# Performance work log

Hardware: AMD Instinct MI355X
Metric: run time of the kernel (lower is better)

The kernel has to match this reference:

```python
import jax, jax.numpy as jnp
import numpy as np

EPS = 1e-8
MARGIN = 0.2
LAMBDA_SM_LSE = 6.0   # i2t attention smooth (opt.lambda_softmax_lse)
LAMBDA_SM_AVG = 9.0   # t2i attention smooth (opt.lambda_softmax_avg)
LAMBDA_LSE = 6.0      # LogSumExp aggregation temperature
NEG = -1e9


def _l2norm(x, axis):
    return x / (jnp.sqrt(jnp.sum(x * x, axis=axis, keepdims=True)) + EPS)


def _cos(a, b):
    # cosine over last axis, torch-style: w12 / clamp(|a||b|, eps)
    w12 = jnp.sum(a * b, axis=-1)
    w1 = jnp.sqrt(jnp.sum(a * a, axis=-1))
    w2 = jnp.sqrt(jnp.sum(b * b, axis=-1))
    return w12 / jnp.maximum(w1 * w2, EPS)


def _forward(im, s, s_l):
    B, R, D = im.shape
    W = s.shape[1]
    wmask = jnp.arange(W)[None, :] < s_l[:, None]          # (Bc, W) valid words
    s = s * wmask[:, :, None]                              # emulate ragged slice s[j,:len_j]

    # ---------------- i2t: query=image regions, context=caption words ----------
    # attn[i,j,w,r] = <s[j,w], im[i,r]>
    A = jnp.einsum('jwd,ird->ijwr', s, im)
    A = jax.nn.leaky_relu(A, 0.1)
    A = _l2norm(A, axis=3)                                 # clipped_l2norm over regions
    logits = jnp.swapaxes(A, 2, 3) * LAMBDA_SM_LSE         # (i,j,r,w), softmax over words
    logits = jnp.where(wmask[None, :, None, :], logits, NEG)
    attn_i2t = jax.nn.softmax(logits, axis=-1)
    wc_t = jnp.einsum('ijrw,jwd->ijrd', attn_i2t, s)       # weighted caption ctx per region
    sim1 = _cos(im[:, None, :, :], wc_t)                   # (i,j,r)
    score1 = jnp.log(jnp.sum(jnp.exp(LAMBDA_LSE * sim1), axis=2)) / LAMBDA_LSE  # (i,j)
    attn_t_full = jnp.mean(wc_t, axis=2)                   # (i,j,d)
    idx = jnp.arange(B)
    attn_t = attn_t_full[idx, idx]                         # (B,d) diagonal

    # ---------------- t2i: query=caption words, context=image regions ----------
    # attn[i,j,r,w] = <im[i,r], s[j,w]>
    Bm = jnp.einsum('ird,jwd->ijrw', im, s)
    Bm = jax.nn.leaky_relu(Bm, 0.1)
    Bm = Bm * wmask[None, :, None, :]                      # padded-word cols excluded from norm
    Bm = _l2norm(Bm, axis=3)                               # clipped_l2norm over words
    logits2 = jnp.swapaxes(Bm, 2, 3) * LAMBDA_SM_AVG       # (i,j,w,r), softmax over regions
    attn_t2i = jax.nn.softmax(logits2, axis=-1)
    wc_i = jnp.einsum('ijwr,ird->ijwd', attn_t2i, im)      # weighted image ctx per word
    sim2 = _cos(s[None, :, :, :], wc_i)                    # (i,j,w)
    e2 = jnp.where(wmask[None, :, :], jnp.exp(LAMBDA_LSE * sim2), 0.0)
    score2 = jnp.log(jnp.sum(e2, axis=2)) / LAMBDA_LSE     # masked LogSumExp over words
    wsum = jnp.sum(wc_i * wmask[None, :, :, None], axis=2)
    attn_i_full = wsum / s_l[None, :, None].astype(wc_i.dtype)  # masked mean over words
    attn_i = attn_i_full[idx, idx]                         # (B,d)

    # ---------------- hinge loss over (B,B) score matrix -----------------------
    scores = 0.5 * (score1 + score2)
    diag = jnp.diagonal(scores)
    cost_s = jnp.maximum(MARGIN + scores - diag[:, None], 0.0)
    cost_im = jnp.maximum(MARGIN + scores - diag[None, :], 0.0)
    eye = jnp.eye(B, dtype=bool)
    cost_s = jnp.where(eye, 0.0, cost_s)
    cost_im = jnp.where(eye, 0.0, cost_im)
    # max_violation=True
    loss = jnp.sum(jnp.max(cost_s, axis=1)) + jnp.sum(jnp.max(cost_im, axis=0))
    return loss, attn_t, attn_i


def setup_inputs() -> dict:
    key = jax.random.key(0)
    k1, k2, k3 = jax.random.split(key, 3)
    B, R, W, D = 64, 36, 40, 1024
    im = jax.random.normal(k1, (B, R, D), dtype=jnp.float32)
    s = jax.random.normal(k2, (B, W, D), dtype=jnp.float32)
    s_l = jax.random.randint(k3, (B,), 10, W + 1)
    return {"im": im, "s": s, "s_l": s_l}


def reference(im, s, s_l):
    return _forward(im, s, s_l)
```

## Files before the change

kernel.cpp:

```cpp
#include <hip/hip_runtime.h>
#include <math.h>

#define Bn 64
#define Rr 36
#define Ww 40
#define Dd 1024
#define GM 2304
#define GN 2560
#define NCONV 4864
#define PAD 72
#define SBP 64
#define EPSf 1e-8f

typedef unsigned short u16;
typedef __attribute__((ext_vector_type(8))) short bf16x8;
typedef __attribute__((ext_vector_type(4))) float f32x4;

struct alignas(8) U16x4 { u16 x, y, z, w; };

__device__ inline u16 f2bf(float x) {
    unsigned int u = __float_as_uint(x);
    u += 0x7FFFu + ((u >> 16) & 1u);
    return (u16)(u >> 16);
}
__device__ inline float bf2f(u16 h) {
    return __uint_as_float(((unsigned int)h) << 16);
}

__device__ __forceinline__ void gl_lds16(const u16* g, u16* l) {
    __builtin_amdgcn_global_load_lds(
        (const __attribute__((address_space(1))) void*)g,
        (__attribute__((address_space(3))) void*)l, 16, 0, 0);
}

__global__ __launch_bounds__(256) void prep_kernel(const float* __restrict__ im,
                                                   const float* __restrict__ s,
                                                   const int* __restrict__ s_l,
                                                   u16* __restrict__ Ab,
                                                   u16* __restrict__ Bb,
                                                   u16* __restrict__ SSb,
                                                   u16* __restrict__ IIb,
                                                   float* __restrict__ SSd,
                                                   float* __restrict__ IId) {
    __shared__ float red[3][64][37];
    int b = blockIdx.x, t = threadIdx.x;
    if (b < NCONV) {
        const int nA4 = GM * Dd / 4;
        int idx = b * 256 + t;
        if (idx < nA4) {
            float4 v = *(const float4*)(im + (size_t)idx * 4);
            U16x4 o = {f2bf(v.x), f2bf(v.y), f2bf(v.z), f2bf(v.w)};
            *(U16x4*)(Ab + (size_t)idx * 4) = o;
        } else {
            int i2 = idx - nA4;
            int f = i2 * 4;
            int row = f >> 10;
            int j = row / Ww, w = row - j * Ww;
            U16x4 o = {0, 0, 0, 0};
            if (w < s_l[j]) {
                float4 v = *(const float4*)(s + (size_t)f);
                o.x = f2bf(v.x); o.y = f2bf(v.y); o.z = f2bf(v.z); o.w = f2bf(v.w);
            }
            *(U16x4*)(Bb + (size_t)i2 * 4) = o;
        }
        return;
    }
    int gb = b - NCONV;
    bool isS = gb < Bn;
    int idx = isS ? gb : gb - Bn;
    int n = isS ? Ww : Rr;
    const float* basef = isS ? (s + (size_t)idx * Ww * Dd) : (im + (size_t)idx * Rr * Dd);
    u16* outb = isS ? (SSb + (size_t)idx * 48 * SBP) : (IIb + (size_t)idx * 48 * SBP);
    float* outd = isS ? (SSd + (size_t)idx * Ww) : (IId + (size_t)idx * Rr);
    int lane = t & 63, wid = t >> 6;
    int frow = lane & 15, fk = (lane >> 4) * 8;

    f32x4 acc[3][3];
    for (int m = 0; m < 3; ++m)
        for (int p = 0; p < 3; ++p) acc[m][p] = (f32x4){0.f, 0.f, 0.f, 0.f};

    for (int ks = 0; ks < 8; ++ks) {
        int k0 = wid * 256 + ks * 32 + fk;
        bf16x8 f[3];
        for (int m = 0; m < 3; ++m) {
            int rr = m * 16 + frow;
            if (rr >= n) rr = n - 1;
            const float* p = basef + (size_t)rr * Dd + k0;
            float4 v0 = *(const float4*)p;
            float4 v1 = *(const float4*)(p + 4);
            bf16x8 fv;
            fv[0] = (short)f2bf(v0.x); fv[1] = (short)f2bf(v0.y);
            fv[2] = (short)f2bf(v0.z); fv[3] = (short)f2bf(v0.w);
            fv[4] = (short)f2bf(v1.x); fv[5] = (short)f2bf(v1.y);
            fv[6] = (short)f2bf(v1.z); fv[7] = (short)f2bf(v1.w);
            f[m] = fv;
        }
        for (int m = 0; m < 3; ++m)
            for (int p = 0; p < 3; ++p)
                acc[m][p] = __builtin_amdgcn_mfma_f32_16x16x32_bf16(f[m], f[p], acc[m][p], 0, 0, 0);
    }
    if (wid) {
        for (int m = 0; m < 3; ++m)
            for (int p = 0; p < 3; ++p)
                for (int q = 0; q < 4; ++q)
                    red[wid - 1][lane][(m * 3 + p) * 4 + q] = acc[m][p][q];
    }
    __syncthreads();
    if (wid == 0) {
        for (int wv = 0; wv < 3; ++wv)
            for (int m = 0; m < 3; ++m)
                for (int p = 0; p < 3; ++p)
                    for (int q = 0; q < 4; ++q)
                        acc[m][p][q] += red[wv][lane][(m * 3 + p) * 4 + q];
        int crow = (lane >> 4) * 4, ccol = lane & 15;
        for (int m = 0; m < 3; ++m)
            for (int p = 0; p < 3; ++p)
                for (int q = 0; q < 4; ++q) {
                    int row = m * 16 + crow + q;
                    int col = p * 16 + ccol;
                    float v = acc[m][p][q];
                    outb[row * SBP + col] = f2bf(v);
                    if (row == col && row < n) outd[row] = v;
                }
    }
}

__global__ __launch_bounds__(256) void gemm_mfma_kernel(const u16* __restrict__ Ab,
                                                        const u16* __restrict__ Bb,
                                                        u16* __restrict__ Gb) {
    __shared__ __align__(16) u16 As[2][64][64];
    __shared__ __align__(16) u16 Bs[2][128][64];
    int bn = blockIdx.x;
    int bm = blockIdx.y;
    int t = threadIdx.x;
    int lane = t & 63, wid = t >> 6;
    int wr = wid >> 1, wc = wid & 1;

    int lrow8 = lane >> 3;
    int sslot = (lane & 7) ^ lrow8;
    const u16* ga = Ab + ((size_t)(bm * 64 + wid * 16) + lrow8) * Dd + sslot * 8;
    const u16* gb = Bb + ((size_t)(bn * 128 + wid * 32) + lrow8) * Dd + sslot * 8;

    f32x4 acc[2][4];
    for (int m = 0; m < 2; ++m)
        for (int n = 0; n < 4; ++n) acc[m][n] = (f32x4){0.f, 0.f, 0.f, 0.f};

    int frow = lane & 15;
    int cgr = lane >> 4;

#define STAGE(BI, KK) do { \
        gl_lds16(ga + (KK), &As[BI][wid * 16][0]); \
        gl_lds16(ga + (size_t)8 * Dd + (KK), &As[BI][wid * 16 + 8][0]); \
        gl_lds16(gb + (KK), &Bs[BI][wid * 32][0]); \
        gl_lds16(gb + (size_t)8 * Dd + (KK), &Bs[BI][wid * 32 + 8][0]); \
        gl_lds16(gb + (size_t)16 * Dd + (KK), &Bs[BI][wid * 32 + 16][0]); \
        gl_lds16(gb + (size_t)24 * Dd + (KK), &Bs[BI][wid * 32 + 24][0]); \
    } while (0)

    STAGE(0, 0);
    for (int step = 0; step < 16; ++step) {
        int cur = step & 1;
        __syncthreads();
        if (step < 15) STAGE(cur ^ 1, (step + 1) * 64);
        bf16x8 af[2][2], bf[4][2];
#pragma unroll
        for (int m = 0; m < 2; ++m) {
            int row = wr * 32 + m * 16 + frow;
#pragma unroll
            for (int ks = 0; ks < 2; ++ks) {
                int slot = (ks * 4 + cgr) ^ (row & 7);
                af[m][ks] = *(const bf16x8*)&As[cur][row][slot * 8];
            }
        }
#pragma unroll
        for (int n = 0; n < 4; ++n) {
            int row = wc * 64 + n * 16 + frow;
#pragma unroll
            for (int ks = 0; ks < 2; ++ks) {
                int slot = (ks * 4 + cgr) ^ (row & 7);
                bf[n][ks] = *(const bf16x8*)&Bs[cur][row][slot * 8];
            }
        }
#pragma unroll
        for (int ks = 0; ks < 2; ++ks)
#pragma unroll
            for (int m = 0; m < 2; ++m)
#pragma unroll
                for (int n = 0; n < 4; ++n)
                    acc[m][n] = __builtin_amdgcn_mfma_f32_16x16x32_bf16(af[m][ks], bf[n][ks], acc[m][n], 0, 0, 0);
    }
#undef STAGE

    int crow0 = bm * 64 + wr * 32 + (lane >> 4) * 4;
    int ccol0 = bn * 128 + wc * 64 + (lane & 15);
    for (int m = 0; m < 2; ++m)
        for (int q = 0; q < 4; ++q) {
            int row = crow0 + m * 16 + q;
            for (int n = 0; n < 4; ++n)
                Gb[(size_t)row * GN + ccol0 + n * 16] = f2bf(acc[m][n][q]);
        }
}

__device__ __forceinline__ void quad_mfma(const u16* att, const u16* M,
                                          float* qout, int nq, int lane) {
    int c = lane & 15, g4 = lane >> 4;
    f32x4 acc[3][3];
#pragma unroll
    for (int m = 0; m < 3; ++m)
#pragma unroll
        for (int p = 0; p < 3; ++p) acc[m][p] = (f32x4){0.f, 0.f, 0.f, 0.f};
#pragma unroll
    for (int ks = 0; ks < 2; ++ks) {
        bf16x8 fa[3], fb[3];
#pragma unroll
        for (int m = 0; m < 3; ++m)
            fa[m] = *(const bf16x8*)&att[(m * 16 + c) * PAD + g4 * 8 + ks * 32];
#pragma unroll
        for (int p = 0; p < 3; ++p)
            fb[p] = *(const bf16x8*)(M + (size_t)(p * 16 + c) * SBP + g4 * 8 + ks * 32);
#pragma unroll
        for (int m = 0; m < 3; ++m)
#pragma unroll
            for (int p = 0; p < 3; ++p)
                acc[m][p] = __builtin_amdgcn_mfma_f32_16x16x32_bf16(fa[m], fb[p], acc[m][p], 0, 0, 0);
    }
#pragma unroll
    for (int m = 0; m < 3; ++m)
#pragma unroll
        for (int q = 0; q < 4; ++q) {
            int row = m * 16 + g4 * 4 + q;
            float sp = 0.f;
#pragma unroll
            for (int p = 0; p < 3; ++p)
                sp += acc[m][p][q] * bf2f(att[row * PAD + p * 16 + c]);
            sp += __shfl_xor(sp, 1);
            sp += __shfl_xor(sp, 2);
            sp += __shfl_xor(sp, 4);
            sp += __shfl_xor(sp, 8);
            if (c == 0 && row < nq) qout[row] = sp;
        }
}

__global__ __launch_bounds__(128) void pair_kernel(const u16* __restrict__ Gb,
                                                   const u16* __restrict__ SSb,
                                                   const u16* __restrict__ IIb,
                                                   const float* __restrict__ SSd,
                                                   const float* __restrict__ IId,
                                                   const int* __restrict__ s_l,
                                                   float* __restrict__ score1,
                                                   float* __restrict__ score2,
                                                   float* __restrict__ dAp,
                                                   float* __restrict__ dBp) {
    int j = blockIdx.x, i = blockIdx.y;
    int t = threadIdx.x, lane = t & 63, wid = t >> 6;
    __shared__ __align__(16) u16 glb[Rr * 44];
    __shared__ __align__(16) u16 attA[48 * PAD];
    __shared__ __align__(16) u16 attB[48 * PAD];
    __shared__ float invA[Ww], invB[Rr], sA[Rr], sB[Ww], qA[Rr], qB[Ww];
    int L = s_l[j];

    {
        uint* za = (uint*)attA;
        uint* zb = (uint*)attB;
#pragma unroll
        for (int k = 0; k < 14; ++k) {
            int idx = t + k * 128;
            if (idx < 48 * PAD / 2) { za[idx] = 0; zb[idx] = 0; }
        }
    }
    float iid = 0.f, ssd = 0.f;
    if (wid == 0 && lane < Rr) {
        iid = IId[i * Rr + lane];
        const u16* gp = Gb + (size_t)(i * Rr + lane) * GN + j * Ww;
        uint2* dst = (uint2*)&glb[lane * 44];
#pragma unroll
        for (int q = 0; q < 5; ++q) {
            uint4 v = *(const uint4*)(gp + q * 8);
            dst[q * 2] = make_uint2(v.x, v.y);
            dst[q * 2 + 1] = make_uint2(v.z, v.w);
        }
    }
    if (wid == 1 && lane < Ww) ssd = SSd[j * Ww + lane];
    __syncthreads();

    if (wid == 0 && lane < Rr) {
        float sum = 0.f;
#pragma unroll 8
        for (int w = 0; w < Ww; ++w) {
            float x = bf2f(glb[lane * 44 + w]);
            x = x < 0.f ? 0.1f * x : x;
            sum += x * x;
        }
        invB[lane] = 9.f / (sqrtf(sum) + EPSf);
    }
    if (wid == 1 && lane < Ww) {
        float sum = 0.f;
#pragma unroll 6
        for (int r = 0; r < Rr; ++r) {
            float x = bf2f(glb[r * 44 + lane]);
            x = x < 0.f ? 0.1f * x : x;
            sum += x * x;
        }
        invA[lane] = 6.f / (sqrtf(sum) + EPSf);
    }
    __syncthreads();

    float dot = 0.f, myinv = 0.f;
    if (wid == 0 && lane < Rr) {
        float ssum = 0.f;
#pragma unroll 8
        for (int w = 0; w < Ww; ++w) {
            float e = 0.f;
            if (w < L) {
                float gx = bf2f(glb[lane * 44 + w]);
                float x = gx < 0.f ? 0.1f * gx : gx;
                e = __expf(x * invA[w]);
                dot += e * gx;
            }
            attA[lane * PAD + w] = f2bf(e);
            ssum += e;
        }
        myinv = 1.f / ssum;
        dot *= myinv;
        sA[lane] = myinv;
    }
    if (wid == 1 && lane < Ww) {
        float ssum = 0.f;
#pragma unroll 6
        for (int r = 0; r < Rr; ++r) {
            float gx = bf2f(glb[r * 44 + lane]);
            float x = gx < 0.f ? 0.1f * gx : gx;
            float e = __expf(x * invB[r]);
            dot += e * gx;
            attB[lane * PAD + r] = f2bf(e);
            ssum += e;
        }
        myinv = 1.f / ssum;
        dot *= myinv;
        sB[lane] = myinv;
    }
    __syncthreads();

    if (wid == 0)
        quad_mfma(attA, SSb + (size_t)j * 48 * SBP, qA, Rr, lane);
    else
        quad_mfma(attB, IIb + (size_t)i * 48 * SBP, qB, Ww, lane);

    if (wid == 0) {
        float e1 = 0.f;
        if (lane < Rr) {
            float q = qA[lane] * myinv * myinv;
            float s1 = dot / fmaxf(sqrtf(iid) * sqrtf(fmaxf(q, 0.f)), EPSf);
            e1 = __expf(6.f * s1);
        }
#pragma unroll
        for (int off = 1; off < 64; off <<= 1) e1 += __shfl_xor(e1, off);
        if (lane == 0) score1[i * Bn + j] = __logf(e1) * (1.f / 6.f);
    } else {
        float e2 = 0.f;
        if (lane < Ww) {
            float q = qB[lane] * myinv * myinv;
            float s2 = dot / fmaxf(sqrtf(ssd) * sqrtf(fmaxf(q, 0.f)), EPSf);
            e2 = (lane < L) ? __expf(6.f * s2) : 0.f;
        }
#pragma unroll
        for (int off = 1; off < 64; off <<= 1) e2 += __shfl_xor(e2, off);
        if (lane == 0) score2[i * Bn + j] = __logf(e2) * (1.f / 6.f);
    }

    if (i == j) {
        __syncthreads();
        if (wid == 1 && lane < Ww) {
            float sum = 0.f;
#pragma unroll 6
            for (int r = 0; r < Rr; ++r) sum += bf2f(attA[r * PAD + lane]) * sA[r];
            dAp[i * Ww + lane] = sum * (1.f / (float)Rr);
        }
        if (wid == 0 && lane < Rr) {
            float sum = 0.f;
            for (int w = 0; w < L; ++w) sum += bf2f(attB[w * PAD + lane]) * sB[w];
            dBp[i * Rr + lane] = sum / (float)L;
        }
    }
}

__global__ __launch_bounds__(256) void diag_out_kernel(const u16* __restrict__ Ab,
                                                       const u16* __restrict__ Bb,
                                                       const int* __restrict__ s_l,
                                                       const float* __restrict__ dA,
                                                       const float* __restrict__ dB,
                                                       const float* __restrict__ score1,
                                                       const float* __restrict__ score2,
                                                       float* __restrict__ out) {
    int t = threadIdx.x;
    if (blockIdx.y == 4) {
        if (blockIdx.x != 0) return;
        __shared__ float sc[Bn][Bn + 1];
        for (int idx = t; idx < Bn * Bn; idx += 256)
            sc[idx >> 6][idx & 63] = 0.5f * (score1[idx] + score2[idx]);
        __syncthreads();
        if (t < 64) {
            float dt = sc[t][t];
            float rowmax = 0.f, colmax = 0.f;
            for (int k = 0; k < Bn; ++k) {
                if (k != t) {
                    rowmax = fmaxf(rowmax, 0.2f + sc[t][k] - dt);
                    colmax = fmaxf(colmax, 0.2f + sc[k][t] - dt);
                }
            }
            float v = rowmax + colmax;
            for (int off = 32; off; off >>= 1) v += __shfl_down(v, off);
            if (t == 0) out[0] = v;
        }
        return;
    }
    int i = blockIdx.x;
    int d = blockIdx.y * 256 + t;
    int L = s_l[i];
    __shared__ float aw[Ww], br[Rr];
    if (t < Ww) aw[t] = dA[i * Ww + t];
    if (t >= 64 && t < 64 + Rr) br[t - 64] = dB[i * Rr + (t - 64)];
    __syncthreads();
    float acc1 = 0.f;
    for (int w = 0; w < L; ++w) acc1 += aw[w] * bf2f(Bb[((size_t)i * Ww + w) * Dd + d]);
    out[1 + (size_t)i * Dd + d] = acc1;
    float acc2 = 0.f;
    for (int r = 0; r < Rr; ++r) acc2 += br[r] * bf2f(Ab[((size_t)i * Rr + r) * Dd + d]);
    out[1 + (size_t)Bn * Dd + (size_t)i * Dd + d] = acc2;
}

extern "C" void kernel_launch(void* const* d_in, const int* in_sizes, int n_in,
                              void* d_out, int out_size, void* d_ws, size_t ws_size,
                              hipStream_t stream) {
    const float* im = (const float*)d_in[0];
    const float* s = (const float*)d_in[1];
    const int* s_l = (const int*)d_in[2];
    float* out = (float*)d_out;

    u16* Ab = (u16*)d_ws;
    u16* Bb = Ab + (size_t)GM * Dd;
    u16* Gb = Bb + (size_t)GN * Dd;
    u16* SSb = Gb + (size_t)GM * GN;
    u16* IIb = SSb + (size_t)Bn * 48 * SBP;
    float* SSd = (float*)(IIb + (size_t)Bn * 48 * SBP);
    float* IId = SSd + (size_t)Bn * Ww;
    float* score1 = IId + (size_t)Bn * Rr;
    float* score2 = score1 + Bn * Bn;
    float* dA = score2 + Bn * Bn;
    float* dB = dA + Bn * Ww;

    prep_kernel<<<NCONV + 2 * Bn, 256, 0, stream>>>(im, s, s_l, Ab, Bb, SSb, IIb, SSd, IId);

    dim3 ggrid(GN / 128, GM / 64);
    gemm_mfma_kernel<<<ggrid, 256, 0, stream>>>(Ab, Bb, Gb);

    dim3 pgrid(Bn, Bn);
    pair_kernel<<<pgrid, 128, 0, stream>>>(Gb, SSb, IIb, SSd, IId, s_l,
                                           score1, score2, dA, dB);

    dim3 dgrid(Bn, 5);
    diag_out_kernel<<<dgrid, 256, 0, stream>>>(Ab, Bb, s_l, dA, dB, score1, score2, out);
}
```

Before: 75.83 us.

## Enlarge GEMM tile to 128x128 with XCD-aware block remap; fuse diag output into pair kernel

The GEMM block tile grows from 64x128 to 128x128, so each wave computes 4x4 MFMA tiles. A 1D grid of 360 blocks is remapped so that neighbouring tiles land on the same XCD, aiming for better operand reuse and fewer block launches. The diagonal context-vector output moves into the i==j blocks of pair_kernel, which removes the dA/dB round trip through global memory, and the loss gets its own tiny kernel. In exchange the GEMM uses more registers and LDS per block, has fewer blocks than CUs, and the diagonal blocks of pair_kernel do serial extra work.

```diff
diff --git a/kernel.cpp b/kernel.cpp
--- a/kernel.cpp
+++ b/kernel.cpp
@@ -128,33 +128,33 @@
 __global__ __launch_bounds__(256) void gemm_mfma_kernel(const u16* __restrict__ Ab,
                                                         const u16* __restrict__ Bb,
                                                         u16* __restrict__ Gb) {
-    __shared__ __align__(16) u16 As[2][64][64];
+    __shared__ __align__(16) u16 As[2][128][64];
     __shared__ __align__(16) u16 Bs[2][128][64];
-    int bn = blockIdx.x;
-    int bm = blockIdx.y;
+    int bid = blockIdx.x;
+    int nb = (bid & 7) * 45 + (bid >> 3);
+    int bn = nb / 18, bm = nb - bn * 18;
     int t = threadIdx.x;
     int lane = t & 63, wid = t >> 6;
     int wr = wid >> 1, wc = wid & 1;
 
     int lrow8 = lane >> 3;
     int sslot = (lane & 7) ^ lrow8;
-    const u16* ga = Ab + ((size_t)(bm * 64 + wid * 16) + lrow8) * Dd + sslot * 8;
+    const u16* ga = Ab + ((size_t)(bm * 128 + wid * 32) + lrow8) * Dd + sslot * 8;
     const u16* gb = Bb + ((size_t)(bn * 128 + wid * 32) + lrow8) * Dd + sslot * 8;
 
-    f32x4 acc[2][4];
-    for (int m = 0; m < 2; ++m)
+    f32x4 acc[4][4];
+    for (int m = 0; m < 4; ++m)
         for (int n = 0; n < 4; ++n) acc[m][n] = (f32x4){0.f, 0.f, 0.f, 0.f};
 
     int frow = lane & 15;
     int cgr = lane >> 4;
 
 #define STAGE(BI, KK) do { \
-        gl_lds16(ga + (KK), &As[BI][wid * 16][0]); \
-        gl_lds16(ga + (size_t)8 * Dd + (KK), &As[BI][wid * 16 + 8][0]); \
-        gl_lds16(gb + (KK), &Bs[BI][wid * 32][0]); \
-        gl_lds16(gb + (size_t)8 * Dd + (KK), &Bs[BI][wid * 32 + 8][0]); \
-        gl_lds16(gb + (size_t)16 * Dd + (KK), &Bs[BI][wid * 32 + 16][0]); \
-        gl_lds16(gb + (size_t)24 * Dd + (KK), &Bs[BI][wid * 32 + 24][0]); \
+        _Pragma("unroll") \
+        for (int r8 = 0; r8 < 4; ++r8) { \
+            gl_lds16(ga + (size_t)(r8 * 8) * Dd + (KK), &As[BI][wid * 32 + r8 * 8][0]); \
+            gl_lds16(gb + (size_t)(r8 * 8) * Dd + (KK), &Bs[BI][wid * 32 + r8 * 8][0]); \
+        } \
     } while (0)
 
     STAGE(0, 0);
@@ -162,10 +162,10 @@
         int cur = step & 1;
         __syncthreads();
         if (step < 15) STAGE(cur ^ 1, (step + 1) * 64);
-        bf16x8 af[2][2], bf[4][2];
-#pragma unroll
-        for (int m = 0; m < 2; ++m) {
-            int row = wr * 32 + m * 16 + frow;
+        bf16x8 af[4][2], bf[4][2];
+#pragma unroll
+        for (int m = 0; m < 4; ++m) {
+            int row = wr * 64 + m * 16 + frow;
 #pragma unroll
             for (int ks = 0; ks < 2; ++ks) {
                 int slot = (ks * 4 + cgr) ^ (row & 7);
@@ -184,16 +184,16 @@
 #pragma unroll
         for (int ks = 0; ks < 2; ++ks)
 #pragma unroll
-            for (int m = 0; m < 2; ++m)
+            for (int m = 0; m < 4; ++m)
 #pragma unroll
                 for (int n = 0; n < 4; ++n)
                     acc[m][n] = __builtin_amdgcn_mfma_f32_16x16x32_bf16(af[m][ks], bf[n][ks], acc[m][n], 0, 0, 0);
     }
 #undef STAGE
 
-    int crow0 = bm * 64 + wr * 32 + (lane >> 4) * 4;
+    int crow0 = bm * 128 + wr * 64 + (lane >> 4) * 4;
     int ccol0 = bn * 128 + wc * 64 + (lane & 15);
-    for (int m = 0; m < 2; ++m)
+    for (int m = 0; m < 4; ++m)
         for (int q = 0; q < 4; ++q) {
             int row = crow0 + m * 16 + q;
             for (int n = 0; n < 4; ++n)
@@ -246,17 +246,19 @@
                                                    const u16* __restrict__ IIb,
                                                    const float* __restrict__ SSd,
                                                    const float* __restrict__ IId,
+                                                   const u16* __restrict__ Ab,
+                                                   const u16* __restrict__ Bb,
                                                    const int* __restrict__ s_l,
                                                    float* __restrict__ score1,
                                                    float* __restrict__ score2,
-                                                   float* __restrict__ dAp,
-                                                   float* __restrict__ dBp) {
+                                                   float* __restrict__ out) {
     int j = blockIdx.x, i = blockIdx.y;
     int t = threadIdx.x, lane = t & 63, wid = t >> 6;
     __shared__ __align__(16) u16 glb[Rr * 44];
     __shared__ __align__(16) u16 attA[48 * PAD];
     __shared__ __align__(16) u16 attB[48 * PAD];
     __shared__ float invA[Ww], invB[Rr], sA[Rr], sB[Ww], qA[Rr], qB[Ww];
+    __shared__ float aw[Ww], br[Rr];
     int L = s_l[j];
 
     {
@@ -374,59 +376,49 @@
             float sum = 0.f;
 #pragma unroll 6
             for (int r = 0; r < Rr; ++r) sum += bf2f(attA[r * PAD + lane]) * sA[r];
-            dAp[i * Ww + lane] = sum * (1.f / (float)Rr);
+            aw[lane] = sum * (1.f / (float)Rr);
         }
         if (wid == 0 && lane < Rr) {
             float sum = 0.f;
             for (int w = 0; w < L; ++w) sum += bf2f(attB[w * PAD + lane]) * sB[w];
-            dBp[i * Rr + lane] = sum / (float)L;
-        }
-    }
-}
-
-__global__ __launch_bounds__(256) void diag_out_kernel(const u16* __restrict__ Ab,
-                                                       const u16* __restrict__ Bb,
-                                                       const int* __restrict__ s_l,
-                                                       const float* __restrict__ dA,
-                                                       const float* __restrict__ dB,
-                                                       const float* __restrict__ score1,
-                                                       const float* __restrict__ score2,
-                                                       float* __restrict__ out) {
+            br[lane] = sum / (float)L;
+        }
+        __syncthreads();
+        const u16* BbI = Bb + (size_t)i * Ww * Dd;
+        const u16* AbI = Ab + (size_t)i * Rr * Dd;
+        for (int d = t; d < Dd; d += 128) {
+            float a1 = 0.f;
+            for (int w = 0; w < L; ++w) a1 += aw[w] * bf2f(BbI[(size_t)w * Dd + d]);
+            out[1 + (size_t)i * Dd + d] = a1;
+            float a2 = 0.f;
+#pragma unroll 6
+            for (int r = 0; r < Rr; ++r) a2 += br[r] * bf2f(AbI[(size_t)r * Dd + d]);
+            out[1 + (size_t)Bn * Dd + (size_t)i * Dd + d] = a2;
+        }
+    }
+}
+
+__global__ void loss_kernel(const float* __restrict__ s1,
+                            const float* __restrict__ s2,
+                            float* __restrict__ out) {
     int t = threadIdx.x;
-    if (blockIdx.y == 4) {
-        if (blockIdx.x != 0) return;
-        __shared__ float sc[Bn][Bn + 1];
-        for (int idx = t; idx < Bn * Bn; idx += 256)
-            sc[idx >> 6][idx & 63] = 0.5f * (score1[idx] + score2[idx]);
-        __syncthreads();
-        if (t < 64) {
-            float dt = sc[t][t];
-            float rowmax = 0.f, colmax = 0.f;
-            for (int k = 0; k < Bn; ++k) {
-                if (k != t) {
-                    rowmax = fmaxf(rowmax, 0.2f + sc[t][k] - dt);
-                    colmax = fmaxf(colmax, 0.2f + sc[k][t] - dt);
-                }
-            }
-            float v = rowmax + colmax;
-            for (int off = 32; off; off >>= 1) v += __shfl_down(v, off);
-            if (t == 0) out[0] = v;
-        }
-        return;
-    }
-    int i = blockIdx.x;
-    int d = blockIdx.y * 256 + t;
-    int L = s_l[i];
-    __shared__ float aw[Ww], br[Rr];
-    if (t < Ww) aw[t] = dA[i * Ww + t];
-    if (t >= 64 && t < 64 + Rr) br[t - 64] = dB[i * Rr + (t - 64)];
+    __shared__ float sc[Bn][Bn + 1];
+    for (int idx = t; idx < Bn * Bn; idx += 64)
+        sc[idx >> 6][idx & 63] = 0.5f * (s1[idx] + s2[idx]);
     __syncthreads();
-    float acc1 = 0.f;
-    for (int w = 0; w < L; ++w) acc1 += aw[w] * bf2f(Bb[((size_t)i * Ww + w) * Dd + d]);
-    out[1 + (size_t)i * Dd + d] = acc1;
-    float acc2 = 0.f;
-    for (int r = 0; r < Rr; ++r) acc2 += br[r] * bf2f(Ab[((size_t)i * Rr + r) * Dd + d]);
-    out[1 + (size_t)Bn * Dd + (size_t)i * Dd + d] = acc2;
+    float dt = sc[t][t];
+    float rowmax = 0.f, colmax = 0.f;
+    for (int k = 0; k < Bn; ++k) {
+        if (k != t) {
+            float cs = 0.2f + sc[t][k] - dt;
+            if (cs > rowmax) rowmax = cs;
+            float ci = 0.2f + sc[k][t] - dt;
+            if (ci > colmax) colmax = ci;
+        }
+    }
+    float v = rowmax + colmax;
+    for (int off = 32; off; off >>= 1) v += __shfl_down(v, off);
+    if (t == 0) out[0] = v;
 }
 
 extern "C" void kernel_launch(void* const* d_in, const int* in_sizes, int n_in,
@@ -446,18 +438,14 @@
     float* IId = SSd + (size_t)Bn * Ww;
     float* score1 = IId + (size_t)Bn * Rr;
     float* score2 = score1 + Bn * Bn;
-    float* dA = score2 + Bn * Bn;
-    float* dB = dA + Bn * Ww;
 
     prep_kernel<<<NCONV + 2 * Bn, 256, 0, stream>>>(im, s, s_l, Ab, Bb, SSb, IIb, SSd, IId);
 
-    dim3 ggrid(GN / 128, GM / 64);
-    gemm_mfma_kernel<<<ggrid, 256, 0, stream>>>(Ab, Bb, Gb);
+    gemm_mfma_kernel<<<360, 256, 0, stream>>>(Ab, Bb, Gb);
 
     dim3 pgrid(Bn, Bn);
-    pair_kernel<<<pgrid, 128, 0, stream>>>(Gb, SSb, IIb, SSd, IId, s_l,
-                                           score1, score2, dA, dB);
-
-    dim3 dgrid(Bn, 5);
-    diag_out_kernel<<<dgrid, 256, 0, stream>>>(Ab, Bb, s_l, dA, dB, score1, score2, out);
-}
+    pair_kernel<<<pgrid, 128, 0, stream>>>(Gb, SSb, IIb, SSd, IId, Ab, Bb, s_l,
+                                           score1, score2, out);
+
+    loss_kernel<<<1, 64, 0, stream>>>(score1, score2, out);
+}
```

After: 120.1 us. 58.3% more time.
